# Optimization experiments

Hardware: AMD Instinct MI355X
Metric: run time of the kernel (lower is better)

The kernel has to match this reference:

```python
import jax, jax.numpy as jnp
import numpy as np

N_NODES = 50000
N_EDGES = 800000
NFEAT, NHID, NCLASS = 128, 256, 64


def setup_inputs() -> dict:
    key = jax.random.key(0)
    ks = jax.random.split(key, 8)
    x = jax.random.normal(ks[0], (N_NODES, NFEAT), dtype=jnp.float32)
    edge_index = jax.random.randint(ks[1], (2, N_EDGES), 0, N_NODES, dtype=jnp.int64)
    s1 = 1.0 / np.sqrt(NFEAT)
    s2 = 1.0 / np.sqrt(NHID)
    W1_neigh = jax.random.normal(ks[2], (NFEAT, NHID), dtype=jnp.float32) * s1
    W1_root = jax.random.normal(ks[3], (NFEAT, NHID), dtype=jnp.float32) * s1
    b1 = jnp.zeros((NHID,), dtype=jnp.float32)
    W2_neigh = jax.random.normal(ks[4], (NHID, NCLASS), dtype=jnp.float32) * s2
    W2_root = jax.random.normal(ks[5], (NHID, NCLASS), dtype=jnp.float32) * s2
    b2 = jnp.zeros((NCLASS,), dtype=jnp.float32)
    return {"x": x, "edge_index": edge_index, "W1_neigh": W1_neigh,
            "W1_root": W1_root, "b1": b1, "W2_neigh": W2_neigh,
            "W2_root": W2_root, "b2": b2}


def _sage_conv(h, src, dst, n_nodes, W_neigh, W_root, b):
    # mean aggregation of source features into destination nodes
    msg = h[src]                                                   # [E, d]
    summed = jax.ops.segment_sum(msg, dst, num_segments=n_nodes)   # [N, d]
    cnt = jax.ops.segment_sum(jnp.ones((src.shape[0],), h.dtype), dst,
                              num_segments=n_nodes)                # [N]
    mean = summed / jnp.maximum(cnt, 1.0)[:, None]
    return mean @ W_neigh + h @ W_root + b


def reference(x, edge_index, W1_neigh, W1_root, b1, W2_neigh, W2_root, b2):
    src, dst = edge_index[0], edge_index[1]
    n = x.shape[0]
    h = jax.nn.relu(_sage_conv(x, src, dst, n, W1_neigh, W1_root, b1))
    # dropout is identity in eval mode
    out = _sage_conv(h, src, dst, n, W2_neigh, W2_root, b2)
    return out
```

## Files before the change

### kernel.cpp

```cpp
#include <hip/hip_runtime.h>

#define N_NODES 50000
#define N_EDGES 800000
#define NFEAT   128
#define NHID    256
#define NCLASS  64

#define NPASS 8
#define PASS_W ((N_NODES + NPASS - 1) / NPASS)
#define ECHUNK ((N_EDGES + 255) / 256)
#define ELLCAP 64

#define CVTX_B ((N_NODES * 32 + 255) / 256)
#define CVTW_B (((65536 + 32768) + 255) / 256)

typedef unsigned short u16;
typedef unsigned int   u32;
typedef __attribute__((ext_vector_type(8))) u16   u16x8;
typedef __attribute__((ext_vector_type(8))) short s16x8;
typedef __attribute__((ext_vector_type(4))) float f32x4;

__device__ inline u16 f2bf(float f) {
    u32 u = __float_as_uint(f);
    u32 r = (u + 0x7FFFu + ((u >> 16) & 1u)) >> 16;
    return (u16)r;
}
__device__ inline float bflo(u32 v) { return __uint_as_float(v << 16); }
__device__ inline float bfhi(u32 v) { return __uint_as_float(v & 0xFFFF0000u); }

#define GLOAD_LDS16(g, l)                                                        \
    __builtin_amdgcn_global_load_lds(                                            \
        (const __attribute__((address_space(1))) u32*)(const void*)(g),          \
        (__attribute__((address_space(3))) u32*)(void*)(l), 16, 0, 0)

__global__ __launch_bounds__(256) void fill_ell_kernel(const int* __restrict__ ei,
                                                       int* __restrict__ cnt,
                                                       int* __restrict__ ell) {
    int p = blockIdx.x & (NPASS - 1);
    int e = (blockIdx.x >> 3) * 256 + threadIdx.x;
    if (e >= N_EDGES) return;
    u32 d = (u32)ei[N_EDGES + e];
    u32 lo = (u32)(p * PASS_W);
    if (d - lo < (u32)PASS_W) {
        int s = ei[e];
        int pos = atomicAdd(&cnt[d], 1);
        if (pos < ELLCAP) ell[(size_t)d * ELLCAP + pos] = s;
    }
}

__global__ __launch_bounds__(256) void prep_kernel(const float* __restrict__ x,
                                                   const float* __restrict__ W1r,
                                                   const float* __restrict__ W1n,
                                                   const float* __restrict__ W2n,
                                                   const float* __restrict__ W2r,
                                                   u16* __restrict__ xa,
                                                   u16* __restrict__ W1t,
                                                   u16* __restrict__ W2t) {
    int b = blockIdx.x;
    if (b < CVTX_B) {
        int idx = b * 256 + threadIdx.x;
        if (idx >= N_NODES * 32) return;
        int r  = idx >> 5;
        int c4 = (idx & 31) * 4;
        float4 v = *reinterpret_cast<const float4*>(x + (size_t)r * NFEAT + c4);
        uint2 o;
        o.x = (u32)f2bf(v.x) | ((u32)f2bf(v.y) << 16);
        o.y = (u32)f2bf(v.z) | ((u32)f2bf(v.w) << 16);
        *reinterpret_cast<uint2*>(xa + (size_t)r * 256 + c4) = o;
    } else {
        int id = (b - CVTX_B) * 256 + threadIdx.x;
        if (id < 65536) {
            int k = id & 255, n = id >> 8;
            float v = (k < NFEAT) ? W1r[(size_t)k * NHID + n]
                                  : W1n[(size_t)(k - NFEAT) * NHID + n];
            W1t[(size_t)n * 256 + k] = f2bf(v);
        } else if (id < 65536 + 32768) {
            int j = id - 65536;
            int k = j & 255, n = j >> 8;
            float v = (n < NCLASS) ? W2n[(size_t)k * NCLASS + n]
                                   : W2r[(size_t)k * NCLASS + (n - NCLASS)];
            W2t[(size_t)n * 256 + k] = f2bf(v);
        }
    }
}

__global__ __launch_bounds__(256) void gather1_kernel(const int* __restrict__ cnt,
                                                      const int* __restrict__ ell,
                                                      u16* __restrict__ xa) {
    int gtid = blockIdx.x * 256 + threadIdx.x;
    int node = gtid >> 6;
    if (node >= N_NODES) return;
    int lane = threadIdx.x & 63;
    const u32* xrow = reinterpret_cast<const u32*>(xa);
    const int* idx = ell + (size_t)node * ELLCAP;
    int deg = cnt[node];
    if (deg > ELLCAP) deg = ELLCAP;
    float ax = 0.0f, ay = 0.0f;
    int j = 0;
    for (; j + 16 <= deg; j += 16) {
        int s[16];
        u32 v[16];
        #pragma unroll
        for (int q = 0; q < 16; ++q) s[q] = idx[j + q];
        #pragma unroll
        for (int q = 0; q < 16; ++q) v[q] = xrow[(size_t)s[q] * 128 + lane];
        #pragma unroll
        for (int q = 0; q < 16; ++q) { ax += bflo(v[q]); ay += bfhi(v[q]); }
    }
    for (; j + 8 <= deg; j += 8) {
        int s[8];
        u32 v[8];
        #pragma unroll
        for (int q = 0; q < 8; ++q) s[q] = idx[j + q];
        #pragma unroll
        for (int q = 0; q < 8; ++q) v[q] = xrow[(size_t)s[q] * 128 + lane];
        #pragma unroll
        for (int q = 0; q < 8; ++q) { ax += bflo(v[q]); ay += bfhi(v[q]); }
    }
    for (; j < deg; ++j) {
        u32 v = xrow[(size_t)idx[j] * 128 + lane];
        ax += bflo(v);
        ay += bfhi(v);
    }
    float invd = 1.0f / fmaxf((float)deg, 1.0f);
    u32 packed = (u32)f2bf(ax * invd) | ((u32)f2bf(ay * invd) << 16);
    reinterpret_cast<u32*>(xa + (size_t)node * 256 + 128)[lane] = packed;
}

__global__ __launch_bounds__(256) void gather2_kernel(const int* __restrict__ cnt,
                                                      const int* __restrict__ ell,
                                                      const u16* __restrict__ t,
                                                      float* __restrict__ out) {
    int gtid = blockIdx.x * 256 + threadIdx.x;
    int wave = gtid >> 6;
    int lane = threadIdx.x & 63;
    int node = wave * 2 + (lane >> 5);
    int l    = lane & 31;
    if (node >= N_NODES) return;
    const u32* trow = reinterpret_cast<const u32*>(t);
    const int* idx = ell + (size_t)node * ELLCAP;
    int deg = cnt[node];
    if (deg > ELLCAP) deg = ELLCAP;
    float ax = 0.0f, ay = 0.0f;
    int j = 0;
    for (; j + 16 <= deg; j += 16) {
        int s[16];
        u32 v[16];
        #pragma unroll
        for (int q = 0; q < 16; ++q) s[q] = idx[j + q];
        #pragma unroll
        for (int q = 0; q < 16; ++q) v[q] = trow[(size_t)s[q] * 32 + l];
        #pragma unroll
        for (int q = 0; q < 16; ++q) { ax += bflo(v[q]); ay += bfhi(v[q]); }
    }
    for (; j + 8 <= deg; j += 8) {
        int s[8];
        u32 v[8];
        #pragma unroll
        for (int q = 0; q < 8; ++q) s[q] = idx[j + q];
        #pragma unroll
        for (int q = 0; q < 8; ++q) v[q] = trow[(size_t)s[q] * 32 + l];
        #pragma unroll
        for (int q = 0; q < 8; ++q) { ax += bflo(v[q]); ay += bfhi(v[q]); }
    }
    for (; j < deg; ++j) {
        u32 v = trow[(size_t)idx[j] * 32 + l];
        ax += bflo(v);
        ay += bfhi(v);
    }
    float invd = 1.0f / fmaxf((float)deg, 1.0f);
    float* o = out + (size_t)node * NCLASS + l * 2;
    o[0] += ax * invd;
    o[1] += ay * invd;
}

__global__ __launch_bounds__(256) void gemm1_mfma(const u16* __restrict__ xa,
                                                  const u16* __restrict__ W1t,
                                                  const float* __restrict__ b1,
                                                  u16* __restrict__ h) {
    __shared__ u16 As[128 * 32];
    __shared__ u16 Bs[128 * 32];
    const int tid = threadIdx.x;
    const int r0 = blockIdx.x * 128;
    const int n0 = blockIdx.y * 128;
    const int wid = tid >> 6, ln = tid & 63;
    const int wm = (wid & 1) * 64, wn = (wid >> 1) * 64;
    const int lr = ln & 15;
    const int lq = ln >> 4;

    f32x4 acc[4][4] = {};

    for (int k0 = 0; k0 < 256; k0 += 32) {
        #pragma unroll
        for (int it = 0; it < 2; ++it) {
            int c   = it * 256 + tid;
            int row = c >> 2;
            int ko  = (c & 3) * 8;
            GLOAD_LDS16(xa  + (size_t)(r0 + row) * 256 + k0 + ko, As + c * 8);
            GLOAD_LDS16(W1t + (size_t)(n0 + row) * 256 + k0 + ko, Bs + c * 8);
        }
        __syncthreads();

        s16x8 af[4], bf[4];
        #pragma unroll
        for (int i = 0; i < 4; ++i)
            af[i] = *reinterpret_cast<const s16x8*>(As + (wm + i * 16 + lr) * 32 + lq * 8);
        #pragma unroll
        for (int j = 0; j < 4; ++j)
            bf[j] = *reinterpret_cast<const s16x8*>(Bs + (wn + j * 16 + lr) * 32 + lq * 8);
        #pragma unroll
        for (int i = 0; i < 4; ++i)
            #pragma unroll
            for (int j = 0; j < 4; ++j)
                acc[i][j] = __builtin_amdgcn_mfma_f32_16x16x32_bf16(af[i], bf[j], acc[i][j], 0, 0, 0);
        __syncthreads();
    }

    #pragma unroll
    for (int i = 0; i < 4; ++i) {
        #pragma unroll
        for (int j = 0; j < 4; ++j) {
            int col = n0 + wn + j * 16 + lr;
            float bias = b1[col];
            #pragma unroll
            for (int r = 0; r < 4; ++r) {
                int row = r0 + wm + i * 16 + lq * 4 + r;
                if (row < N_NODES)
                    h[(size_t)row * 256 + col] = f2bf(fmaxf(acc[i][j][r] + bias, 0.0f));
            }
        }
    }
}

__global__ __launch_bounds__(256) void gemm2_mfma(const u16* __restrict__ h,
                                                  const u16* __restrict__ W2t,
                                                  const float* __restrict__ b2,
                                                  u16* __restrict__ t,
                                                  float* __restrict__ out) {
    __shared__ u16 As[128 * 32];
    __shared__ u16 Bs[128 * 32];
    const int tid = threadIdx.x;
    const int r0 = blockIdx.x * 128;
    const int wid = tid >> 6, ln = tid & 63;
    const int wm = (wid & 1) * 64, wn = (wid >> 1) * 64;
    const int lr = ln & 15;
    const int lq = ln >> 4;

    f32x4 acc[4][4] = {};

    for (int k0 = 0; k0 < 256; k0 += 32) {
        #pragma unroll
        for (int it = 0; it < 2; ++it) {
            int c   = it * 256 + tid;
            int row = c >> 2;
            int ko  = (c & 3) * 8;
            GLOAD_LDS16(h   + (size_t)(r0 + row) * 256 + k0 + ko, As + c * 8);
            GLOAD_LDS16(W2t + (size_t)row * 256 + k0 + ko,        Bs + c * 8);
        }
        __syncthreads();

        s16x8 af[4], bf[4];
        #pragma unroll
        for (int i = 0; i < 4; ++i)
            af[i] = *reinterpret_cast<const s16x8*>(As + (wm + i * 16 + lr) * 32 + lq * 8);
        #pragma unroll
        for (int j = 0; j < 4; ++j)
            bf[j] = *reinterpret_cast<const s16x8*>(Bs + (wn + j * 16 + lr) * 32 + lq * 8);
        #pragma unroll
        for (int i = 0; i < 4; ++i)
            #pragma unroll
            for (int j = 0; j < 4; ++j)
                acc[i][j] = __builtin_amdgcn_mfma_f32_16x16x32_bf16(af[i], bf[j], acc[i][j], 0, 0, 0);
        __syncthreads();
    }

    #pragma unroll
    for (int i = 0; i < 4; ++i) {
        #pragma unroll
        for (int j = 0; j < 4; ++j) {
            int col = wn + j * 16 + lr;
            #pragma unroll
            for (int r = 0; r < 4; ++r) {
                int row = r0 + wm + i * 16 + lq * 4 + r;
                if (row >= N_NODES) continue;
                if (col < NCLASS) {
                    t[(size_t)row * NCLASS + col] = f2bf(acc[i][j][r]);
                } else {
                    int c = col - NCLASS;
                    out[(size_t)row * NCLASS + c] = acc[i][j][r] + b2[c];
                }
            }
        }
    }
}

extern "C" void kernel_launch(void* const* d_in, const int* in_sizes, int n_in,
                              void* d_out, int out_size, void* d_ws, size_t ws_size,
                              hipStream_t stream) {
    const float* x    = (const float*)d_in[0];
    const int*   ei   = (const int*)d_in[1];
    const float* W1n  = (const float*)d_in[2];
    const float* W1r  = (const float*)d_in[3];
    const float* b1   = (const float*)d_in[4];
    const float* W2n  = (const float*)d_in[5];
    const float* W2r  = (const float*)d_in[6];
    const float* b2   = (const float*)d_in[7];
    float* out = (float*)d_out;

    int* cnt = (int*)d_ws;
    int* ell = cnt + 50048;
    u16* xa  = (u16*)(ell + (size_t)N_NODES * ELLCAP);
    u16* h   = xa + (size_t)N_NODES * 256;
    u16* t   = h  + (size_t)N_NODES * 256;
    u16* W1t = t  + (size_t)N_NODES * 64;
    u16* W2t = W1t + 65536;

    hipMemsetAsync(cnt, 0, 50048 * sizeof(int), stream);

    fill_ell_kernel<<<ECHUNK * NPASS, 256, 0, stream>>>(ei, cnt, ell);

    prep_kernel<<<CVTX_B + CVTW_B, 256, 0, stream>>>(x, W1r, W1n, W2n, W2r, xa, W1t, W2t);

    gather1_kernel<<<(N_NODES * 64 + 255) / 256, 256, 0, stream>>>(cnt, ell, xa);
    gemm1_mfma<<<dim3((N_NODES + 127) / 128, 2), 256, 0, stream>>>(xa, W1t, b1, h);

    gemm2_mfma<<<(N_NODES + 127) / 128, 256, 0, stream>>>(h, W2t, b2, t, out);
    gather2_kernel<<<(N_NODES * 32 + 255) / 256, 256, 0, stream>>>(cnt, ell, t, out);
}
```

Measured before the change: 232.9 us.

## Fuse first-layer neighbor gather into GEMM1 and merge ELL fill with prep

The layer-1 mean aggregation is moved inside the GEMM1 kernel. Each block gathers its 128 nodes' neighbor means into shared memory and uses them directly as the second half of the K dimension, so the aggregated features are never written to and re-read from global memory. Each GEMM1 block now covers all 256 output columns instead of splitting them across two blocks, which removes the second pass over the A tile. The ELL-building pass is merged into the conversion kernel to cut one launch. In exchange, the gather runs with far fewer waves (four per block, 32 nodes each, serially) and with large shared-memory and register use, which lowers occupancy for a latency-bound gather.

Measured after the change: 289.9 us. +24.5%, slower.

```diff
diff --git a/kernel.cpp b/kernel.cpp
--- a/kernel.cpp
+++ b/kernel.cpp
@@ -11,6 +11,7 @@
 #define ECHUNK ((N_EDGES + 255) / 256)
 #define ELLCAP 64
 
+#define FILL_B (ECHUNK * NPASS)
 #define CVTX_B ((N_NODES * 32 + 255) / 256)
 #define CVTW_B (((65536 + 32768) + 255) / 256)
 
@@ -33,32 +34,31 @@
         (const __attribute__((address_space(1))) u32*)(const void*)(g),          \
         (__attribute__((address_space(3))) u32*)(void*)(l), 16, 0, 0)
 
-__global__ __launch_bounds__(256) void fill_ell_kernel(const int* __restrict__ ei,
-                                                       int* __restrict__ cnt,
-                                                       int* __restrict__ ell) {
-    int p = blockIdx.x & (NPASS - 1);
-    int e = (blockIdx.x >> 3) * 256 + threadIdx.x;
-    if (e >= N_EDGES) return;
-    u32 d = (u32)ei[N_EDGES + e];
-    u32 lo = (u32)(p * PASS_W);
-    if (d - lo < (u32)PASS_W) {
-        int s = ei[e];
-        int pos = atomicAdd(&cnt[d], 1);
-        if (pos < ELLCAP) ell[(size_t)d * ELLCAP + pos] = s;
-    }
-}
-
-__global__ __launch_bounds__(256) void prep_kernel(const float* __restrict__ x,
-                                                   const float* __restrict__ W1r,
-                                                   const float* __restrict__ W1n,
-                                                   const float* __restrict__ W2n,
-                                                   const float* __restrict__ W2r,
-                                                   u16* __restrict__ xa,
-                                                   u16* __restrict__ W1t,
-                                                   u16* __restrict__ W2t) {
+__global__ __launch_bounds__(256) void prep_fill_kernel(const float* __restrict__ x,
+                                                        const int* __restrict__ ei,
+                                                        const float* __restrict__ W1r,
+                                                        const float* __restrict__ W1n,
+                                                        const float* __restrict__ W2n,
+                                                        const float* __restrict__ W2r,
+                                                        u16* __restrict__ xa,
+                                                        int* __restrict__ cnt,
+                                                        int* __restrict__ ell,
+                                                        u16* __restrict__ W1t,
+                                                        u16* __restrict__ W2t) {
     int b = blockIdx.x;
-    if (b < CVTX_B) {
-        int idx = b * 256 + threadIdx.x;
+    if (b < FILL_B) {
+        int p = b & (NPASS - 1);
+        int e = (b >> 3) * 256 + threadIdx.x;
+        if (e >= N_EDGES) return;
+        u32 d = (u32)ei[N_EDGES + e];
+        u32 lo = (u32)(p * PASS_W);
+        if (d - lo < (u32)PASS_W) {
+            int s = ei[e];
+            int pos = atomicAdd(&cnt[d], 1);
+            if (pos < ELLCAP) ell[(size_t)d * ELLCAP + pos] = s;
+        }
+    } else if (b < FILL_B + CVTX_B) {
+        int idx = (b - FILL_B) * 256 + threadIdx.x;
         if (idx >= N_NODES * 32) return;
         int r  = idx >> 5;
         int c4 = (idx & 31) * 4;
@@ -66,9 +66,9 @@
         uint2 o;
         o.x = (u32)f2bf(v.x) | ((u32)f2bf(v.y) << 16);
         o.y = (u32)f2bf(v.z) | ((u32)f2bf(v.w) << 16);
-        *reinterpret_cast<uint2*>(xa + (size_t)r * 256 + c4) = o;
+        *reinterpret_cast<uint2*>(xa + (size_t)r * 128 + c4) = o;
     } else {
-        int id = (b - CVTX_B) * 256 + threadIdx.x;
+        int id = (b - FILL_B - CVTX_B) * 256 + threadIdx.x;
         if (id < 65536) {
             int k = id & 255, n = id >> 8;
             float v = (k < NFEAT) ? W1r[(size_t)k * NHID + n]
@@ -84,47 +84,181 @@
     }
 }
 
-__global__ __launch_bounds__(256) void gather1_kernel(const int* __restrict__ cnt,
-                                                      const int* __restrict__ ell,
-                                                      u16* __restrict__ xa) {
-    int gtid = blockIdx.x * 256 + threadIdx.x;
-    int node = gtid >> 6;
-    if (node >= N_NODES) return;
-    int lane = threadIdx.x & 63;
-    const u32* xrow = reinterpret_cast<const u32*>(xa);
-    const int* idx = ell + (size_t)node * ELLCAP;
-    int deg = cnt[node];
-    if (deg > ELLCAP) deg = ELLCAP;
-    float ax = 0.0f, ay = 0.0f;
-    int j = 0;
-    for (; j + 16 <= deg; j += 16) {
-        int s[16];
-        u32 v[16];
-        #pragma unroll
-        for (int q = 0; q < 16; ++q) s[q] = idx[j + q];
-        #pragma unroll
-        for (int q = 0; q < 16; ++q) v[q] = xrow[(size_t)s[q] * 128 + lane];
-        #pragma unroll
-        for (int q = 0; q < 16; ++q) { ax += bflo(v[q]); ay += bfhi(v[q]); }
-    }
-    for (; j + 8 <= deg; j += 8) {
-        int s[8];
-        u32 v[8];
-        #pragma unroll
-        for (int q = 0; q < 8; ++q) s[q] = idx[j + q];
-        #pragma unroll
-        for (int q = 0; q < 8; ++q) v[q] = xrow[(size_t)s[q] * 128 + lane];
-        #pragma unroll
-        for (int q = 0; q < 8; ++q) { ax += bflo(v[q]); ay += bfhi(v[q]); }
-    }
-    for (; j < deg; ++j) {
-        u32 v = xrow[(size_t)idx[j] * 128 + lane];
-        ax += bflo(v);
-        ay += bfhi(v);
-    }
-    float invd = 1.0f / fmaxf((float)deg, 1.0f);
-    u32 packed = (u32)f2bf(ax * invd) | ((u32)f2bf(ay * invd) << 16);
-    reinterpret_cast<u32*>(xa + (size_t)node * 256 + 128)[lane] = packed;
+__global__ __launch_bounds__(256) void gemm1_fused(const u16* __restrict__ xa,
+                                                   const int* __restrict__ cnt,
+                                                   const int* __restrict__ ell,
+                                                   const u16* __restrict__ W1t,
+                                                   const float* __restrict__ b1,
+                                                   u16* __restrict__ h) {
+    __shared__ u16 As[128 * 32];
+    __shared__ u16 Bs[256 * 32];
+    __shared__ u32 Gs[128 * 68];
+    const int tid = threadIdx.x;
+    const int r0 = blockIdx.x * 128;
+    const int wid = tid >> 6, ln = tid & 63;
+    const int lr = ln & 15;
+    const int lq = ln >> 4;
+
+    {
+        const u32* xrow = reinterpret_cast<const u32*>(xa);
+        for (int n = 0; n < 32; ++n) {
+            int row = wid * 32 + n;
+            int node = r0 + row;
+            if (node >= N_NODES) break;
+            const int* idx = ell + (size_t)node * ELLCAP;
+            int deg = cnt[node];
+            if (deg > ELLCAP) deg = ELLCAP;
+            float ax = 0.0f, ay = 0.0f;
+            int j = 0;
+            for (; j + 16 <= deg; j += 16) {
+                int s[16]; u32 v[16];
+                #pragma unroll
+                for (int q = 0; q < 16; ++q) s[q] = idx[j + q];
+                #pragma unroll
+                for (int q = 0; q < 16; ++q) v[q] = xrow[(size_t)s[q] * 64 + ln];
+                #pragma unroll
+                for (int q = 0; q < 16; ++q) { ax += bflo(v[q]); ay += bfhi(v[q]); }
+            }
+            for (; j + 8 <= deg; j += 8) {
+                int s[8]; u32 v[8];
+                #pragma unroll
+                for (int q = 0; q < 8; ++q) s[q] = idx[j + q];
+                #pragma unroll
+                for (int q = 0; q < 8; ++q) v[q] = xrow[(size_t)s[q] * 64 + ln];
+                #pragma unroll
+                for (int q = 0; q < 8; ++q) { ax += bflo(v[q]); ay += bfhi(v[q]); }
+            }
+            for (; j < deg; ++j) {
+                u32 v = xrow[(size_t)idx[j] * 64 + ln];
+                ax += bflo(v); ay += bfhi(v);
+            }
+            float invd = 1.0f / fmaxf((float)deg, 1.0f);
+            Gs[row * 68 + ln] = (u32)f2bf(ax * invd) | ((u32)f2bf(ay * invd) << 16);
+        }
+    }
+    __syncthreads();
+
+    const int wm = (wid & 1) * 64;
+    const int wn = (wid >> 1) * 128;
+    f32x4 acc[4][8] = {};
+
+    for (int k0 = 0; k0 < 256; k0 += 32) {
+        if (k0 < 128) {
+            #pragma unroll
+            for (int it = 0; it < 2; ++it) {
+                int c   = it * 256 + tid;
+                int row = c >> 2;
+                int ko  = (c & 3) * 8;
+                GLOAD_LDS16(xa + (size_t)(r0 + row) * 128 + k0 + ko, As + c * 8);
+            }
+        }
+        #pragma unroll
+        for (int it = 0; it < 4; ++it) {
+            int c   = it * 256 + tid;
+            int row = c >> 2;
+            int ko  = (c & 3) * 8;
+            GLOAD_LDS16(W1t + (size_t)row * 256 + k0 + ko, Bs + c * 8);
+        }
+        __syncthreads();
+
+        s16x8 af[4], bf[8];
+        if (k0 < 128) {
+            #pragma unroll
+            for (int i = 0; i < 4; ++i)
+                af[i] = *reinterpret_cast<const s16x8*>(As + (wm + i * 16 + lr) * 32 + lq * 8);
+        } else {
+            #pragma unroll
+            for (int i = 0; i < 4; ++i)
+                af[i] = *reinterpret_cast<const s16x8*>(
+                    (const u16*)(Gs + (size_t)(wm + i * 16 + lr) * 68 + ((k0 - 128) >> 1) + lq * 4));
+        }
+        #pragma unroll
+        for (int j = 0; j < 8; ++j)
+            bf[j] = *reinterpret_cast<const s16x8*>(Bs + (wn + j * 16 + lr) * 32 + lq * 8);
+        #pragma unroll
+        for (int i = 0; i < 4; ++i)
+            #pragma unroll
+            for (int j = 0; j < 8; ++j)
+                acc[i][j] = __builtin_amdgcn_mfma_f32_16x16x32_bf16(af[i], bf[j], acc[i][j], 0, 0, 0);
+        __syncthreads();
+    }
+
+    #pragma unroll
+    for (int i = 0; i < 4; ++i) {
+        #pragma unroll
+        for (int j = 0; j < 8; ++j) {
+            int col = wn + j * 16 + lr;
+            float bias = b1[col];
+            #pragma unroll
+            for (int r = 0; r < 4; ++r) {
+                int row = r0 + wm + i * 16 + lq * 4 + r;
+                if (row < N_NODES)
+                    h[(size_t)row * 256 + col] = f2bf(fmaxf(acc[i][j][r] + bias, 0.0f));
+            }
+        }
+    }
+}
+
+__global__ __launch_bounds__(256) void gemm2_mfma(const u16* __restrict__ h,
+                                                  const u16* __restrict__ W2t,
+                                                  const float* __restrict__ b2,
+                                                  u16* __restrict__ t,
+                                                  float* __restrict__ out) {
+    __shared__ u16 As[128 * 32];
+    __shared__ u16 Bs[128 * 32];
+    const int tid = threadIdx.x;
+    const int r0 = blockIdx.x * 128;
+    const int wid = tid >> 6, ln = tid & 63;
+    const int wm = (wid & 1) * 64, wn = (wid >> 1) * 64;
+    const int lr = ln & 15;
+    const int lq = ln >> 4;
+
+    f32x4 acc[4][4] = {};
+
+    for (int k0 = 0; k0 < 256; k0 += 32) {
+        #pragma unroll
+        for (int it = 0; it < 2; ++it) {
+            int c   = it * 256 + tid;
+            int row = c >> 2;
+            int ko  = (c & 3) * 8;
+            GLOAD_LDS16(h   + (size_t)(r0 + row) * 256 + k0 + ko, As + c * 8);
+            GLOAD_LDS16(W2t + (size_t)row * 256 + k0 + ko,        Bs + c * 8);
+        }
+        __syncthreads();
+
+        s16x8 af[4], bf[4];
+        #pragma unroll
+        for (int i = 0; i < 4; ++i)
+            af[i] = *reinterpret_cast<const s16x8*>(As + (wm + i * 16 + lr) * 32 + lq * 8);
+        #pragma unroll
+        for (int j = 0; j < 4; ++j)
+            bf[j] = *reinterpret_cast<const s16x8*>(Bs + (wn + j * 16 + lr) * 32 + lq * 8);
+        #pragma unroll
+        for (int i = 0; i < 4; ++i)
+            #pragma unroll
+            for (int j = 0; j < 4; ++j)
+                acc[i][j] = __builtin_amdgcn_mfma_f32_16x16x32_bf16(af[i], bf[j], acc[i][j], 0, 0, 0);
+        __syncthreads();
+    }
+
+    #pragma unroll
+    for (int i = 0; i < 4; ++i) {
+        #pragma unroll
+        for (int j = 0; j < 4; ++j) {
+            int col = wn + j * 16 + lr;
+            #pragma unroll
+            for (int r = 0; r < 4; ++r) {
+                int row = r0 + wm + i * 16 + lq * 4 + r;
+                if (row >= N_NODES) continue;
+                if (col < NCLASS) {
+                    t[(size_t)row * NCLASS + col] = f2bf(acc[i][j][r]);
+                } else {
+                    int c = col - NCLASS;
+                    out[(size_t)row * NCLASS + c] = acc[i][j][r] + b2[c];
+                }
+            }
+        }
+    }
 }
 
 __global__ __launch_bounds__(256) void gather2_kernel(const int* __restrict__ cnt,
@@ -144,8 +278,7 @@
     float ax = 0.0f, ay = 0.0f;
     int j = 0;
     for (; j + 16 <= deg; j += 16) {
-        int s[16];
-        u32 v[16];
+        int s[16]; u32 v[16];
         #pragma unroll
         for (int q = 0; q < 16; ++q) s[q] = idx[j + q];
         #pragma unroll
@@ -154,8 +287,7 @@
         for (int q = 0; q < 16; ++q) { ax += bflo(v[q]); ay += bfhi(v[q]); }
     }
     for (; j + 8 <= deg; j += 8) {
-        int s[8];
-        u32 v[8];
+        int s[8]; u32 v[8];
         #pragma unroll
         for (int q = 0; q < 8; ++q) s[q] = idx[j + q];
         #pragma unroll
@@ -165,133 +297,12 @@
     }
     for (; j < deg; ++j) {
         u32 v = trow[(size_t)idx[j] * 32 + l];
-        ax += bflo(v);
-        ay += bfhi(v);
+        ax += bflo(v); ay += bfhi(v);
     }
     float invd = 1.0f / fmaxf((float)deg, 1.0f);
     float* o = out + (size_t)node * NCLASS + l * 2;
     o[0] += ax * invd;
     o[1] += ay * invd;
-}
-
-__global__ __launch_bounds__(256) void gemm1_mfma(const u16* __restrict__ xa,
-                                                  const u16* __restrict__ W1t,
-                                                  const float* __restrict__ b1,
-                                                  u16* __restrict__ h) {
-    __shared__ u16 As[128 * 32];
-    __shared__ u16 Bs[128 * 32];
-    const int tid = threadIdx.x;
-    const int r0 = blockIdx.x * 128;
-    const int n0 = blockIdx.y * 128;
-    const int wid = tid >> 6, ln = tid & 63;
-    const int wm = (wid & 1) * 64, wn = (wid >> 1) * 64;
-    const int lr = ln & 15;
-    const int lq = ln >> 4;
-
-    f32x4 acc[4][4] = {};
-
-    for (int k0 = 0; k0 < 256; k0 += 32) {
-        #pragma unroll
-        for (int it = 0; it < 2; ++it) {
-            int c   = it * 256 + tid;
-            int row = c >> 2;
-            int ko  = (c & 3) * 8;
-            GLOAD_LDS16(xa  + (size_t)(r0 + row) * 256 + k0 + ko, As + c * 8);
-            GLOAD_LDS16(W1t + (size_t)(n0 + row) * 256 + k0 + ko, Bs + c * 8);
-        }
-        __syncthreads();
-
-        s16x8 af[4], bf[4];
-        #pragma unroll
-        for (int i = 0; i < 4; ++i)
-            af[i] = *reinterpret_cast<const s16x8*>(As + (wm + i * 16 + lr) * 32 + lq * 8);
-        #pragma unroll
-        for (int j = 0; j < 4; ++j)
-            bf[j] = *reinterpret_cast<const s16x8*>(Bs + (wn + j * 16 + lr) * 32 + lq * 8);
-        #pragma unroll
-        for (int i = 0; i < 4; ++i)
-            #pragma unroll
-            for (int j = 0; j < 4; ++j)
-                acc[i][j] = __builtin_amdgcn_mfma_f32_16x16x32_bf16(af[i], bf[j], acc[i][j], 0, 0, 0);
-        __syncthreads();
-    }
-
-    #pragma unroll
-    for (int i = 0; i < 4; ++i) {
-        #pragma unroll
-        for (int j = 0; j < 4; ++j) {
-            int col = n0 + wn + j * 16 + lr;
-            float bias = b1[col];
-            #pragma unroll
-            for (int r = 0; r < 4; ++r) {
-                int row = r0 + wm + i * 16 + lq * 4 + r;
-                if (row < N_NODES)
-                    h[(size_t)row * 256 + col] = f2bf(fmaxf(acc[i][j][r] + bias, 0.0f));
-            }
-        }
-    }
-}
-
-__global__ __launch_bounds__(256) void gemm2_mfma(const u16* __restrict__ h,
-                                                  const u16* __restrict__ W2t,
-                                                  const float* __restrict__ b2,
-                                                  u16* __restrict__ t,
-                                                  float* __restrict__ out) {
-    __shared__ u16 As[128 * 32];
-    __shared__ u16 Bs[128 * 32];
-    const int tid = threadIdx.x;
-    const int r0 = blockIdx.x * 128;
-    const int wid = tid >> 6, ln = tid & 63;
-    const int wm = (wid & 1) * 64, wn = (wid >> 1) * 64;
-    const int lr = ln & 15;
-    const int lq = ln >> 4;
-
-    f32x4 acc[4][4] = {};
-
-    for (int k0 = 0; k0 < 256; k0 += 32) {
-        #pragma unroll
-        for (int it = 0; it < 2; ++it) {
-            int c   = it * 256 + tid;
-            int row = c >> 2;
-            int ko  = (c & 3) * 8;
-            GLOAD_LDS16(h   + (size_t)(r0 + row) * 256 + k0 + ko, As + c * 8);
-            GLOAD_LDS16(W2t + (size_t)row * 256 + k0 + ko,        Bs + c * 8);
-        }
-        __syncthreads();
-
-        s16x8 af[4], bf[4];
-        #pragma unroll
-        for (int i = 0; i < 4; ++i)
-            af[i] = *reinterpret_cast<const s16x8*>(As + (wm + i * 16 + lr) * 32 + lq * 8);
-        #pragma unroll
-        for (int j = 0; j < 4; ++j)
-            bf[j] = *reinterpret_cast<const s16x8*>(Bs + (wn + j * 16 + lr) * 32 + lq * 8);
-        #pragma unroll
-        for (int i = 0; i < 4; ++i)
-            #pragma unroll
-            for (int j = 0; j < 4; ++j)
-                acc[i][j] = __builtin_amdgcn_mfma_f32_16x16x32_bf16(af[i], bf[j], acc[i][j], 0, 0, 0);
-        __syncthreads();
-    }
-
-    #pragma unroll
-    for (int i = 0; i < 4; ++i) {
-        #pragma unroll
-        for (int j = 0; j < 4; ++j) {
-            int col = wn + j * 16 + lr;
-            #pragma unroll
-            for (int r = 0; r < 4; ++r) {
-                int row = r0 + wm + i * 16 + lq * 4 + r;
-                if (row >= N_NODES) continue;
-                if (col < NCLASS) {
-                    t[(size_t)row * NCLASS + col] = f2bf(acc[i][j][r]);
-                } else {
-                    int c = col - NCLASS;
-                    out[(size_t)row * NCLASS + c] = acc[i][j][r] + b2[c];
-                }
-            }
-        }
-    }
 }
 
 extern "C" void kernel_launch(void* const* d_in, const int* in_sizes, int n_in,
@@ -310,19 +321,17 @@
     int* cnt = (int*)d_ws;
     int* ell = cnt + 50048;
     u16* xa  = (u16*)(ell + (size_t)N_NODES * ELLCAP);
-    u16* h   = xa + (size_t)N_NODES * 256;
+    u16* h   = xa + (size_t)N_NODES * 128;
     u16* t   = h  + (size_t)N_NODES * 256;
     u16* W1t = t  + (size_t)N_NODES * 64;
     u16* W2t = W1t + 65536;
 
     hipMemsetAsync(cnt, 0, 50048 * sizeof(int), stream);
 
-    fill_ell_kernel<<<ECHUNK * NPASS, 256, 0, stream>>>(ei, cnt, ell);
-
-    prep_kernel<<<CVTX_B + CVTW_B, 256, 0, stream>>>(x, W1r, W1n, W2n, W2r, xa, W1t, W2t);
-
-    gather1_kernel<<<(N_NODES * 64 + 255) / 256, 256, 0, stream>>>(cnt, ell, xa);
-    gemm1_mfma<<<dim3((N_NODES + 127) / 128, 2), 256, 0, stream>>>(xa, W1t, b1, h);
+    prep_fill_kernel<<<FILL_B + CVTX_B + CVTW_B, 256, 0, stream>>>(
+        x, ei, W1r, W1n, W2n, W2r, xa, cnt, ell, W1t, W2t);
+
+    gemm1_fused<<<(N_NODES + 127) / 128, 256, 0, stream>>>(xa, cnt, ell, W1t, b1, h);
 
     gemm2_mfma<<<(N_NODES + 127) / 128, 256, 0, stream>>>(h, W2t, b2, t, out);
     gather2_kernel<<<(N_NODES * 32 + 255) / 256, 256, 0, stream>>>(cnt, ell, t, out);
```
